# Kernel optimization log

Measured on AMD Instinct MI355X. Metric: run time of the kernel, lower is better.

The kernel has to match this reference:

```python
import jax, jax.numpy as jnp
import numpy as np

# Model hyperparameters (match init_kwargs)
B, REF_P, IN_P, OUT_P = 32, 256, 256, 256
K, KS = 4, 3
RATIO = 0.25
HIDDEN = int(REF_P * RATIO) + 1  # 65, per canonical attention1d
TEMP = 34.0
STRIDE, PAD, DIL, GROUPS = 1, 1, 1, 1
L, L_REF = 4096, 64


def setup_inputs() -> dict:
    key = jax.random.key(0)
    k0, k1, k2, k3, k4 = jax.random.split(key, 5)
    ref = jax.random.normal(k0, (B, REF_P, L_REF), dtype=jnp.float32)
    x = jax.random.normal(k1, (B, IN_P, L), dtype=jnp.float32)
    # attention1d params: fc1 (1x1 conv, no bias), fc2 (1x1 conv, with bias)
    att_w1 = jax.random.normal(k2, (HIDDEN, REF_P), dtype=jnp.float32) * (1.0 / np.sqrt(REF_P))
    att_w2 = jax.random.normal(k3, (K, HIDDEN), dtype=jnp.float32) * (1.0 / np.sqrt(HIDDEN))
    att_b2 = jnp.zeros((K,), dtype=jnp.float32)
    # kaiming-uniform-ish K-bank of conv kernels: [K, out, in/groups, ks]
    fan_in = (IN_P // GROUPS) * KS
    bound = np.sqrt(6.0 / fan_in)
    weight = jax.random.uniform(k4, (K, OUT_P, IN_P // GROUPS, KS), dtype=jnp.float32,
                                minval=-bound, maxval=bound)
    bias = jnp.zeros((K, OUT_P), dtype=jnp.float32)
    return {"ref": ref, "x": x, "att_w1": att_w1, "att_w2": att_w2,
            "att_b2": att_b2, "weight": weight, "bias": bias}


def reference(ref, x, att_w1, att_w2, att_b2, weight, bias):
    b = x.shape[0]
    # attention1d: global avg pool over length, two 1x1 convs, softmax w/ temperature
    pooled = jnp.mean(ref, axis=-1)                       # [B, REF_P]
    h = jax.nn.relu(pooled @ att_w1.T)                    # [B, HIDDEN]
    logits = h @ att_w2.T + att_b2                        # [B, K]
    attn = jax.nn.softmax(logits / TEMP, axis=1)          # [B, K]
    # aggregate per-sample kernel bank
    agg_w = jnp.einsum('bk,koic->boic', attn, weight)     # [B, OUT, IN/g, KS]
    agg_b = attn @ bias                                   # [B, OUT]
    # batched grouped conv1d, exactly as F.conv1d with groups=B*GROUPS
    xr = x.reshape(1, b * IN_P, -1)                       # [1, B*IN, L]
    wr = agg_w.reshape(b * OUT_P, IN_P // GROUPS, KS)     # [B*OUT, IN/g, KS]
    out = jax.lax.conv_general_dilated(
        xr, wr, window_strides=(STRIDE,), padding=[(PAD, PAD)],
        rhs_dilation=(DIL,), dimension_numbers=('NCH', 'OIH', 'NCH'),
        feature_group_count=b * GROUPS)                   # [1, B*OUT, L_out]
    out = out.reshape(b, OUT_P, -1) + agg_b[:, :, None]
    return out
```

## Files before the change

### kernel.cpp

```cpp
#include <hip/hip_runtime.h>
#include <cstdint>
#include <cstddef>

typedef __bf16 bf16;
typedef bf16 bf16x8 __attribute__((ext_vector_type(8)));
typedef float f32x4 __attribute__((ext_vector_type(4)));

typedef __attribute__((address_space(1))) void as1_void;
typedef __attribute__((address_space(3))) void as3_void;

__device__ __forceinline__ void gload16(const void* g, void* l) {
  __builtin_amdgcn_global_load_lds((const as1_void*)g, (as3_void*)l, 16, 0, 0);
}
#define SBAR()   __builtin_amdgcn_s_barrier()
#define LGKM0()  do { asm volatile("s_waitcnt lgkmcnt(0)" ::: "memory"); \
                      __builtin_amdgcn_sched_barrier(0); } while (0)
#define VMCNT(n) asm volatile("s_waitcnt vmcnt(" #n ")" ::: "memory")

__global__ __launch_bounds__(256) void attn_kernel(
    const float* __restrict__ ref, const float* __restrict__ w1,
    const float* __restrict__ w2, const float* __restrict__ b2,
    const float* __restrict__ bias, float* __restrict__ attn,
    float* __restrict__ aggb) {
  const int b = blockIdx.x, t = threadIdx.x;
  __shared__ float pooled[256];
  __shared__ float hsh[65];
  __shared__ float ash[4];
  {
    const float* r = ref + ((size_t)b * 256 + t) * 64;
    float s = 0.f;
    #pragma unroll
    for (int l = 0; l < 64; l += 4) {
      float4 v = *(const float4*)(r + l);
      s += v.x + v.y + v.z + v.w;
    }
    pooled[t] = s * (1.0f / 64.0f);
  }
  __syncthreads();
  if (t < 65) {
    const float* w = w1 + t * 256;
    float s = 0.f;
    for (int p = 0; p < 256; ++p) s += pooled[p] * w[p];
    hsh[t] = fmaxf(s, 0.f);
  }
  __syncthreads();
  if (t == 0) {
    float lg[4];
    for (int k = 0; k < 4; ++k) {
      float s = b2[k];
      for (int j = 0; j < 65; ++j) s += hsh[j] * w2[k * 65 + j];
      lg[k] = s * (1.0f / 34.0f);
    }
    float m = fmaxf(fmaxf(lg[0], lg[1]), fmaxf(lg[2], lg[3]));
    float e[4], se = 0.f;
    for (int k = 0; k < 4; ++k) { e[k] = expf(lg[k] - m); se += e[k]; }
    float inv = 1.0f / se;
    for (int k = 0; k < 4; ++k) { float a = e[k] * inv; ash[k] = a; attn[b * 4 + k] = a; }
  }
  __syncthreads();
  {
    float s = 0.f;
    for (int k = 0; k < 4; ++k) s += ash[k] * bias[k * 256 + t];
    aggb[b * 256 + t] = s;
  }
}

__global__ __launch_bounds__(256) void aggw_kernel(
    const float* __restrict__ weight, const float* __restrict__ attn,
    bf16* __restrict__ Wagg) {
  const int o = blockIdx.x, b = blockIdx.y, i = threadIdx.x;
  const float a0 = attn[b * 4 + 0], a1 = attn[b * 4 + 1];
  const float a2 = attn[b * 4 + 2], a3 = attn[b * 4 + 3];
  const size_t ks = (size_t)256 * 256 * 3;
  const float* w = weight + ((size_t)o * 256 + i) * 3;
  bf16* dst = Wagg + ((size_t)(b * 256 + o)) * 768 + i;
  #pragma unroll
  for (int s = 0; s < 3; ++s) {
    float v = a0 * w[s] + a1 * w[ks + s] + a2 * w[2 * ks + s] + a3 * w[3 * ks + s];
    dst[s * 256] = (bf16)v;
  }
}

__global__ __launch_bounds__(512) void conv_kernel(
    const float* __restrict__ x, const bf16* __restrict__ Wagg,
    const float* __restrict__ aggb, float* __restrict__ out) {
  __shared__ bf16 Wl[3][256 * 64];
  __shared__ bf16 Xl[258 * 64];
  const int tid = threadIdx.x;
  const int lane = tid & 63, wid = tid >> 6;
  const int bid = blockIdx.x;
  const int swz = (bid & 7) * 64 + (bid >> 3);
  const int b  = swz >> 4;
  const int lt = swz & 15;
  const int l0 = lt * 256;
  const int wm = wid >> 2, wn = wid & 3;
  const float* xb = x + (size_t)b * 256 * 4096;
  const bf16* Wb = Wagg + (size_t)b * 256 * 768;
  f32x4 acc[8][4] = {};

  auto stage_w_half = [&](int slice, int half) {
    const int ss = slice % 3, ibb = slice / 3;
    const int koff = ss * 256 + ibb * 64;
    char* base = (char*)&Wl[slice % 3][0];
    #pragma unroll
    for (int r = half * 2; r < half * 2 + 2; ++r) {
      int c = r * 512 + tid;
      int row = c >> 3, subg = (c & 7) ^ (row & 7);
      gload16(Wb + (size_t)row * 768 + koff + subg * 8,
              base + (r * 512 + wid * 64) * 16);
    }
  };

  const int sg = tid >> 6, lq = tid & 63;
  const float* xq = xb + ((size_t)sg * 8) * 4096 + l0 + lq * 4;
  const int ei = tid >> 1;
  const int erow = (tid & 1) ? 257 : 0;
  const int el = (tid & 1) ? (l0 + 256) : (l0 - 1);
  const bool edge_ok = (el >= 0) && (el < 4096);
  float4 xv[8];
  float ev = 0.f;

  auto load_x = [&](int ib) {
    const float* p = xq + (size_t)ib * 64 * 4096;
    #pragma unroll
    for (int r = 0; r < 8; ++r)
      xv[r] = *(const float4*)(p + (size_t)r * 4096);
    if (tid < 128)
      ev = edge_ok ? xb[(size_t)(ib * 64 + ei) * 4096 + el] : 0.f;
  };
  auto write_x = [&]() {
    char* base = (char*)&Xl[0];
    #pragma unroll
    for (int q = 0; q < 4; ++q) {
      const int row = lq * 4 + 1 + q;
      bf16x8 pk;
      #pragma unroll
      for (int r = 0; r < 8; ++r) pk[r] = (bf16)(((const float*)&xv[r])[q]);
      *(bf16x8*)(base + row * 128 + ((sg ^ (row & 7)) << 4)) = pk;
    }
    if (tid < 128)
      *(bf16*)(base + erow * 128 + (((ei >> 3) ^ (erow & 7)) << 4) + (ei & 7) * 2)
          = (bf16)ev;
  };

  load_x(0);
  write_x();
  stage_w_half(0, 0); stage_w_half(0, 1);
  stage_w_half(1, 0); stage_w_half(1, 1);
  LGKM0();
  VMCNT(4);
  SBAR();

  for (int t = 0; t < 12; ++t) {
    const int s = t % 3, ib = t / 3;
    const char* wbuf = (const char*)&Wl[t % 3][0];
    const char* xbuf = (const char*)&Xl[0];
    #pragma unroll
    for (int kk = 0; kk < 2; ++kk) {
      const int sub = (lane >> 4) + kk * 4;
      bf16x8 af[8], bfr[4];
      #pragma unroll
      for (int j = 0; j < 8; ++j) {
        int row = wm * 128 + j * 16 + (lane & 15);
        af[j] = *(const bf16x8*)(wbuf + row * 128 + ((sub ^ (row & 7)) << 4));
      }
      #pragma unroll
      for (int n = 0; n < 4; ++n) {
        int row = wn * 64 + n * 16 + (lane & 15) + s;
        bfr[n] = *(const bf16x8*)(xbuf + row * 128 + ((sub ^ (row & 7)) << 4));
      }
      if (t < 10) stage_w_half(t + 2, kk);
      if (kk == 1 && s == 2 && ib < 3) load_x(ib + 1);
      SBAR();
      LGKM0();
      __builtin_amdgcn_s_setprio(1);
      #pragma unroll
      for (int j = 0; j < 8; ++j)
        #pragma unroll
        for (int n = 0; n < 4; ++n)
          acc[j][n] = __builtin_amdgcn_mfma_f32_16x16x32_bf16(af[j], bfr[n], acc[j][n], 0, 0, 0);
      __builtin_amdgcn_s_setprio(0);
      if (kk == 0) {
        SBAR();
      } else if (s < 2) {
        if (t == 10) { VMCNT(0); } else { VMCNT(4); }
        SBAR();
      } else if (t < 11) {
        SBAR();
        write_x();
        LGKM0();
        SBAR();
      }
    }
  }

  const int b256 = b * 256;
  #pragma unroll
  for (int j = 0; j < 8; ++j) {
    const int ob = wm * 128 + j * 16 + ((lane >> 4) << 2);
    float bb[4];
    #pragma unroll
    for (int r = 0; r < 4; ++r) bb[r] = aggb[b256 + ob + r];
    #pragma unroll
    for (int n = 0; n < 4; ++n) {
      const int l = l0 + wn * 64 + n * 16 + (lane & 15);
      f32x4 v = acc[j][n];
      #pragma unroll
      for (int r = 0; r < 4; ++r)
        out[((size_t)(b256 + ob + r)) * 4096 + l] = v[r] + bb[r];
    }
  }
}

extern "C" void kernel_launch(void* const* d_in, const int* in_sizes, int n_in,
                              void* d_out, int out_size, void* d_ws, size_t ws_size,
                              hipStream_t stream) {
  const float* ref    = (const float*)d_in[0];
  const float* x      = (const float*)d_in[1];
  const float* w1     = (const float*)d_in[2];
  const float* w2     = (const float*)d_in[3];
  const float* b2     = (const float*)d_in[4];
  const float* weight = (const float*)d_in[5];
  const float* bias   = (const float*)d_in[6];
  float* out = (float*)d_out;
  char* ws = (char*)d_ws;

  const size_t WAGG_BYTES = (size_t)32 * 256 * 768 * 2;
  bf16* Wagg  = (bf16*)ws;
  float* attn = (float*)(ws + WAGG_BYTES);
  float* aggb = (float*)(ws + WAGG_BYTES + 512);

  attn_kernel<<<32, 256, 0, stream>>>(ref, w1, w2, b2, bias, attn, aggb);
  aggw_kernel<<<dim3(256, 32), 256, 0, stream>>>(weight, attn, Wagg);
  conv_kernel<<<512, 512, 0, stream>>>(x, Wagg, aggb, out);
}
```

Before: 101.0 us.

## Use 128x128 warp tiles with 256-thread blocks and double-buffered weights

The conv kernel drops from 8 to 4 waves per block, and each wave now computes a 128x128 output tile with an 8x8 grid of MFMA accumulators. The goal is more operand reuse per LDS fragment load. The triple-buffered weight staging with hand-placed vmcnt, lgkmcnt and s_barrier waits becomes a double buffer synchronised by plain __syncthreads, and each thread loads twice as many x rows. The cost is much higher register pressure (256 accumulator registers per lane), half as many waves to hide latency, and coarser synchronisation that overlaps memory and compute less.

```diff
diff --git a/kernel.cpp b/kernel.cpp
--- a/kernel.cpp
+++ b/kernel.cpp
@@ -12,10 +12,6 @@
 __device__ __forceinline__ void gload16(const void* g, void* l) {
   __builtin_amdgcn_global_load_lds((const as1_void*)g, (as3_void*)l, 16, 0, 0);
 }
-#define SBAR()   __builtin_amdgcn_s_barrier()
-#define LGKM0()  do { asm volatile("s_waitcnt lgkmcnt(0)" ::: "memory"); \
-                      __builtin_amdgcn_sched_barrier(0); } while (0)
-#define VMCNT(n) asm volatile("s_waitcnt vmcnt(" #n ")" ::: "memory")
 
 __global__ __launch_bounds__(256) void attn_kernel(
     const float* __restrict__ ref, const float* __restrict__ w1,
@@ -81,10 +77,10 @@
   }
 }
 
-__global__ __launch_bounds__(512) void conv_kernel(
+__global__ __launch_bounds__(256) void conv_kernel(
     const float* __restrict__ x, const bf16* __restrict__ Wagg,
     const float* __restrict__ aggb, float* __restrict__ out) {
-  __shared__ bf16 Wl[3][256 * 64];
+  __shared__ bf16 Wl[2][256 * 64];
   __shared__ bf16 Xl[258 * 64];
   const int tid = threadIdx.x;
   const int lane = tid & 63, wid = tid >> 6;
@@ -93,38 +89,43 @@
   const int b  = swz >> 4;
   const int lt = swz & 15;
   const int l0 = lt * 256;
-  const int wm = wid >> 2, wn = wid & 3;
+  const int wm = wid >> 1, wn = wid & 1;
   const float* xb = x + (size_t)b * 256 * 4096;
   const bf16* Wb = Wagg + (size_t)b * 256 * 768;
-  f32x4 acc[8][4] = {};
-
-  auto stage_w_half = [&](int slice, int half) {
-    const int ss = slice % 3, ibb = slice / 3;
+  f32x4 acc[8][8] = {};
+
+  auto stage_w = [&](int t, int buf) {
+    const int ss = t % 3, ibb = t / 3;
     const int koff = ss * 256 + ibb * 64;
-    char* base = (char*)&Wl[slice % 3][0];
-    #pragma unroll
-    for (int r = half * 2; r < half * 2 + 2; ++r) {
-      int c = r * 512 + tid;
+    char* base = (char*)&Wl[buf][0];
+    #pragma unroll
+    for (int inst = 0; inst < 8; ++inst) {
+      int c = inst * 256 + tid;
       int row = c >> 3, subg = (c & 7) ^ (row & 7);
       gload16(Wb + (size_t)row * 768 + koff + subg * 8,
-              base + (r * 512 + wid * 64) * 16);
+              base + (inst * 256 + wid * 64) * 16);
     }
   };
 
-  const int sg = tid >> 6, lq = tid & 63;
-  const float* xq = xb + ((size_t)sg * 8) * 4096 + l0 + lq * 4;
+  const int lq = tid & 63;
+  const int sg = tid >> 6;
+  const float* xqA = xb + ((size_t)sg * 8) * 4096 + l0 + lq * 4;
+  const float* xqB = xb + ((size_t)(sg + 4) * 8) * 4096 + l0 + lq * 4;
   const int ei = tid >> 1;
   const int erow = (tid & 1) ? 257 : 0;
   const int el = (tid & 1) ? (l0 + 256) : (l0 - 1);
   const bool edge_ok = (el >= 0) && (el < 4096);
-  float4 xv[8];
+  float4 xvA[8], xvB[8];
   float ev = 0.f;
 
   auto load_x = [&](int ib) {
-    const float* p = xq + (size_t)ib * 64 * 4096;
-    #pragma unroll
-    for (int r = 0; r < 8; ++r)
-      xv[r] = *(const float4*)(p + (size_t)r * 4096);
+    const float* pA = xqA + (size_t)ib * 64 * 4096;
+    const float* pB = xqB + (size_t)ib * 64 * 4096;
+    #pragma unroll
+    for (int r = 0; r < 8; ++r) {
+      xvA[r] = *(const float4*)(pA + (size_t)r * 4096);
+      xvB[r] = *(const float4*)(pB + (size_t)r * 4096);
+    }
     if (tid < 128)
       ev = edge_ok ? xb[(size_t)(ib * 64 + ei) * 4096 + el] : 0.f;
   };
@@ -133,10 +134,14 @@
     #pragma unroll
     for (int q = 0; q < 4; ++q) {
       const int row = lq * 4 + 1 + q;
-      bf16x8 pk;
+      bf16x8 pkA, pkB;
       #pragma unroll
-      for (int r = 0; r < 8; ++r) pk[r] = (bf16)(((const float*)&xv[r])[q]);
-      *(bf16x8*)(base + row * 128 + ((sg ^ (row & 7)) << 4)) = pk;
+      for (int r = 0; r < 8; ++r) {
+        pkA[r] = (bf16)(((const float*)&xvA[r])[q]);
+        pkB[r] = (bf16)(((const float*)&xvB[r])[q]);
+      }
+      *(bf16x8*)(base + row * 128 + ((sg ^ (row & 7)) << 4)) = pkA;
+      *(bf16x8*)(base + row * 128 + (((sg + 4) ^ (row & 7)) << 4)) = pkB;
     }
     if (tid < 128)
       *(bf16*)(base + erow * 128 + (((ei >> 3) ^ (erow & 7)) << 4) + (ei & 7) * 2)
@@ -144,53 +149,44 @@
   };
 
   load_x(0);
+  stage_w(0, 0);
+  stage_w(1, 1);
   write_x();
-  stage_w_half(0, 0); stage_w_half(0, 1);
-  stage_w_half(1, 0); stage_w_half(1, 1);
-  LGKM0();
-  VMCNT(4);
-  SBAR();
-
-  for (int t = 0; t < 12; ++t) {
-    const int s = t % 3, ib = t / 3;
-    const char* wbuf = (const char*)&Wl[t % 3][0];
-    const char* xbuf = (const char*)&Xl[0];
-    #pragma unroll
-    for (int kk = 0; kk < 2; ++kk) {
-      const int sub = (lane >> 4) + kk * 4;
-      bf16x8 af[8], bfr[4];
+  __syncthreads();
+
+  for (int J = 0; J < 4; ++J) {
+    #pragma unroll
+    for (int s = 0; s < 3; ++s) {
+      const int t = J * 3 + s;
+      const char* wbuf = (const char*)&Wl[(J + s) & 1][0];
+      const char* xbuf = (const char*)&Xl[0];
+      if (t < 11) stage_w(t + 1, (t + 1) & 1);
+      if (s == 2 && J < 3) load_x(J + 1);
       #pragma unroll
-      for (int j = 0; j < 8; ++j) {
-        int row = wm * 128 + j * 16 + (lane & 15);
-        af[j] = *(const bf16x8*)(wbuf + row * 128 + ((sub ^ (row & 7)) << 4));
+      for (int kk = 0; kk < 2; ++kk) {
+        const int sub = (lane >> 4) + kk * 4;
+        bf16x8 af[8], bfr[8];
+        #pragma unroll
+        for (int j = 0; j < 8; ++j) {
+          int row = wm * 128 + j * 16 + (lane & 15);
+          af[j] = *(const bf16x8*)(wbuf + row * 128 + ((sub ^ (row & 7)) << 4));
+        }
+        #pragma unroll
+        for (int n = 0; n < 8; ++n) {
+          int row = wn * 128 + n * 16 + (lane & 15) + s;
+          bfr[n] = *(const bf16x8*)(xbuf + row * 128 + ((sub ^ (row & 7)) << 4));
+        }
+        #pragma unroll
+        for (int j = 0; j < 8; ++j)
+          #pragma unroll
+          for (int n = 0; n < 8; ++n)
+            acc[j][n] = __builtin_amdgcn_mfma_f32_16x16x32_bf16(af[j], bfr[n], acc[j][n], 0, 0, 0);
       }
-      #pragma unroll
-      for (int n = 0; n < 4; ++n) {
-        int row = wn * 64 + n * 16 + (lane & 15) + s;
-        bfr[n] = *(const bf16x8*)(xbuf + row * 128 + ((sub ^ (row & 7)) << 4));
-      }
-      if (t < 10) stage_w_half(t + 2, kk);
-      if (kk == 1 && s == 2 && ib < 3) load_x(ib + 1);
-      SBAR();
-      LGKM0();
-      __builtin_amdgcn_s_setprio(1);
-      #pragma unroll
-      for (int j = 0; j < 8; ++j)
-        #pragma unroll
-        for (int n = 0; n < 4; ++n)
-          acc[j][n] = __builtin_amdgcn_mfma_f32_16x16x32_bf16(af[j], bfr[n], acc[j][n], 0, 0, 0);
-      __builtin_amdgcn_s_setprio(0);
-      if (kk == 0) {
-        SBAR();
-      } else if (s < 2) {
-        if (t == 10) { VMCNT(0); } else { VMCNT(4); }
-        SBAR();
-      } else if (t < 11) {
-        SBAR();
-        write_x();
-        LGKM0();
-        SBAR();
-      }
+      if (t < 11) __syncthreads();
+    }
+    if (J < 3) {
+      write_x();
+      __syncthreads();
     }
   }
 
@@ -202,8 +198,8 @@
     #pragma unroll
     for (int r = 0; r < 4; ++r) bb[r] = aggb[b256 + ob + r];
     #pragma unroll
-    for (int n = 0; n < 4; ++n) {
-      const int l = l0 + wn * 64 + n * 16 + (lane & 15);
+    for (int n = 0; n < 8; ++n) {
+      const int l = l0 + wn * 128 + n * 16 + (lane & 15);
       f32x4 v = acc[j][n];
       #pragma unroll
       for (int r = 0; r < 4; ++r)
@@ -232,5 +228,5 @@
 
   attn_kernel<<<32, 256, 0, stream>>>(ref, w1, w2, b2, bias, attn, aggb);
   aggw_kernel<<<dim3(256, 32), 256, 0, stream>>>(weight, attn, Wagg);
-  conv_kernel<<<512, 512, 0, stream>>>(x, Wagg, aggb, out);
-}
+  conv_kernel<<<512, 256, 0, stream>>>(x, Wagg, aggb, out);
+}
```

Result: slower. 110.5 us (+9.4%).
